# Kernel optimization log

Hardware: AMD Instinct MI355X
Metric: run time of the kernel (lower is better)

The kernel has to match this reference:

```python
import jax, jax.numpy as jnp
import numpy as np

NUM_NODES = 50000
NUM_EDGES = 1600000
NUM_GRAPHS = 64
K_HOPS = 3


def setup_inputs() -> dict:
    key = jax.random.key(0)
    ks = jax.random.split(key, 8)
    d_in, d_h, d_out = 128, 512, 16
    x = jax.random.normal(ks[0], (NUM_NODES, d_in), dtype=jnp.float32)
    edge_index = jax.random.randint(ks[1], (2, NUM_EDGES), 0, NUM_NODES, dtype=jnp.int64)
    batch = jnp.sort(jax.random.randint(ks[2], (NUM_NODES,), 0, NUM_GRAPHS, dtype=jnp.int64))
    w1 = jax.random.normal(ks[3], (d_in, d_h), dtype=jnp.float32) / np.sqrt(d_in)
    b1 = jnp.zeros((d_h,), dtype=jnp.float32)
    w2 = jax.random.normal(ks[4], (d_h, d_h), dtype=jnp.float32) / np.sqrt(d_h)
    b2 = jnp.zeros((d_h,), dtype=jnp.float32)
    wc = jax.random.normal(ks[5], (d_h, d_out), dtype=jnp.float32) / np.sqrt(d_h)
    bc = jnp.zeros((d_out,), dtype=jnp.float32)
    return {"x": x, "edge_index": edge_index, "batch": batch,
            "w1": w1, "b1": b1, "w2": w2, "b2": b2, "wc": wc, "bc": bc}


def _propagate(x, row, col, norm):
    # one hop: out[r] += x[c] * norm  (degree-normalized scatter-add)
    msg = x[col] * norm[:, None]                      # [E+N, d]
    return jax.ops.segment_sum(msg, row, num_segments=NUM_NODES)


def reference(x, edge_index, batch, w1, b1, w2, b2, wc, bc):
    # add self loops
    loops = jnp.arange(NUM_NODES, dtype=edge_index.dtype)
    row = jnp.concatenate([edge_index[0], loops])
    col = jnp.concatenate([edge_index[1], loops])
    deg = jax.ops.segment_sum(jnp.ones_like(row, dtype=jnp.float32), row,
                              num_segments=NUM_NODES)
    deg = jnp.clip(deg, 1.0)
    norm = 1.0 / deg[row]                             # [E+N]
    # K-hop propagation (eval mode: dropout / drop_node inactive)
    h = x
    for _ in range(K_HOPS):
        h = _propagate(h, row, col, norm)
    # MLP
    h = jax.nn.relu(h @ w1 + b1)
    h = h @ w2 + b2
    # global mean pool over graphs
    sums = jax.ops.segment_sum(h, batch, num_segments=NUM_GRAPHS)
    cnts = jax.ops.segment_sum(jnp.ones((h.shape[0],), dtype=h.dtype), batch,
                               num_segments=NUM_GRAPHS)
    pooled = sums / jnp.clip(cnts, 1.0)[:, None]      # [G, d_h]
    return pooled @ wc + bc                            # [G, out]
```

## Files before the change

kernel.cpp:

```cpp
#include <hip/hip_runtime.h>
#include <hip/hip_bf16.h>
#include <hip/hip_fp8.h>

#define N_NODES 50000
#define N_EDGES 1600000
#define N_GRAPHS 64
#define D_IN 128
#define D_H 512
#define D_OUT 16

#define NBUK 391
#define BUK_CAP 4608
#define P1_EDGES 4096
#define P1_BLOCKS ((N_EDGES + P1_EDGES - 1) / P1_EDGES)

#define MSPLIT 8

typedef short bf16x8 __attribute__((ext_vector_type(8)));
typedef float f32x4 __attribute__((ext_vector_type(4)));

static __device__ __forceinline__ unsigned short f2bf(float f) {
    __hip_bfloat16 h = __float2bfloat16(f);
    return *(unsigned short*)&h;
}

static __device__ __forceinline__ float2 fp8x2_dec(unsigned short u) {
    __hip_fp8x2_e4m3 p;
    p.__x = (__hip_fp8x2_storage_t)u;
    return static_cast<float2>(p);
}

static __device__ __forceinline__ unsigned short fp8x2_enc(float a, float b) {
    __hip_fp8_e4m3 pa(a), pb(b);
    return (unsigned short)((unsigned)pa.__x | ((unsigned)pb.__x << 8));
}

static __device__ __forceinline__ void dec16_add(uint4 u, float* acc) {
    unsigned vv[4] = {u.x, u.y, u.z, u.w};
#pragma unroll
    for (int w = 0; w < 4; ++w) {
        float2 a = fp8x2_dec((unsigned short)(vv[w] & 0xFFFFu));
        float2 b = fp8x2_dec((unsigned short)(vv[w] >> 16));
        acc[w * 4 + 0] += a.x; acc[w * 4 + 1] += a.y;
        acc[w * 4 + 2] += b.x; acc[w * 4 + 3] += b.y;
    }
}


__global__ __launch_bounds__(512) void partition_edges(const int* __restrict__ row,
                                                       const int* __restrict__ col,
                                                       int* __restrict__ bucket_cnt,
                                                       unsigned* __restrict__ edge_buf) {
    __shared__ unsigned recs[P1_EDGES];
    __shared__ unsigned sorted[P1_EDGES];
    __shared__ int hist4[4][NBUK];
    __shared__ int cur4[4][NBUK];
    __shared__ int gbase[NBUK];
    __shared__ int scan[512];
    int tid = threadIdx.x;
    int w2 = tid >> 7;
    int e0 = blockIdx.x * P1_EDGES;
    int m = N_EDGES - e0; if (m > P1_EDGES) m = P1_EDGES;

    for (int i = tid; i < 4 * NBUK; i += 512) ((int*)hist4)[i] = 0;
    for (int i = tid; i < 4 * NBUK; i += 512) ((int*)cur4)[i] = 0;
    __syncthreads();
    for (int i = tid; i < m; i += 512) {
        int r = row[e0 + i];
        int c = col[e0 + i];
        int buk = r >> 7;
        recs[i] = ((unsigned)buk << 23) | ((unsigned)(r & 127) << 16) | (unsigned)c;
        atomicAdd(&hist4[w2][buk], 1);
    }
    __syncthreads();
    int tot = 0;
    if (tid < NBUK) tot = hist4[0][tid] + hist4[1][tid] + hist4[2][tid] + hist4[3][tid];
    scan[tid] = (tid < NBUK) ? tot : 0;
    __syncthreads();
    for (int off = 1; off < 512; off <<= 1) {
        int v = (tid >= off) ? scan[tid - off] : 0;
        __syncthreads();
        scan[tid] += v;
        __syncthreads();
    }
    if (tid < NBUK) {
        int run = (tid == 0) ? 0 : scan[tid - 1];
        gbase[tid] = (tot > 0) ? atomicAdd(&bucket_cnt[tid], tot) : 0;
#pragma unroll
        for (int w = 0; w < 4; ++w) {
            int c = hist4[w][tid];
            hist4[w][tid] = run;
            run += c;
        }
    }
    __syncthreads();
    for (int i = tid; i < m; i += 512) {
        unsigned rec = recs[i];
        int buk = rec >> 23;
        int rank = atomicAdd(&cur4[w2][buk], 1);
        sorted[hist4[w2][buk] + rank] = rec;
    }
    __syncthreads();
    for (int p = tid; p < m; p += 512) {
        unsigned rec = sorted[p];
        int buk = rec >> 23;
        edge_buf[(size_t)buk * BUK_CAP + gbase[buk] + (p - hist4[0][buk])] = rec;
    }
}

__global__ __launch_bounds__(512) void finalize_csr(const unsigned* __restrict__ edge_buf,
                                                    const int* __restrict__ bucket_cnt,
                                                    int* __restrict__ rowptr,
                                                    float* __restrict__ invdeg,
                                                    unsigned short* __restrict__ csr_col) {
    __shared__ int hist[128], excl[128], cur[128];
    __shared__ int scan[512];
    int b = blockIdx.x;
    int tid = threadIdx.x;
    scan[tid] = (tid < NBUK) ? bucket_cnt[tid] : 0;
    __syncthreads();
    for (int off = 1; off < 512; off <<= 1) {
        int v = (tid >= off) ? scan[tid - off] : 0;
        __syncthreads();
        scan[tid] += v;
        __syncthreads();
    }
    int cnt = bucket_cnt[b];
    int base = (b == 0) ? 0 : scan[b - 1];
    const unsigned* src = edge_buf + (size_t)b * BUK_CAP;
    __syncthreads();
    if (tid < 128) { hist[tid] = 0; cur[tid] = 0; }
    __syncthreads();
    for (int i = tid; i < cnt; i += 512)
        atomicAdd(&hist[(src[i] >> 16) & 127], 1);
    __syncthreads();
    scan[tid] = (tid < 128) ? hist[tid] : 0;
    __syncthreads();
    for (int off = 1; off < 512; off <<= 1) {
        int v = (tid >= off) ? scan[tid - off] : 0;
        __syncthreads();
        scan[tid] += v;
        __syncthreads();
    }
    if (tid < 128) excl[tid] = (tid == 0) ? 0 : scan[tid - 1];
    __syncthreads();
    int r = b * 128 + tid;
    if (tid < 128 && r < N_NODES) {
        rowptr[r] = base + excl[tid];
        invdeg[r] = 1.0f / (float)(hist[tid] + 1);
    }
    if (b == NBUK - 1 && tid == 0) rowptr[N_NODES] = base + cnt;
    for (int i = tid; i < cnt; i += 512) {
        unsigned rec = src[i];
        int rl = (rec >> 16) & 127;
        int pos = excl[rl] + atomicAdd(&cur[rl], 1);
        csr_col[base + pos] = (unsigned short)(rec & 0xFFFFu);
    }
}


__global__ __launch_bounds__(256) void prep(const float* __restrict__ x,
                                            unsigned short* __restrict__ xf,
                                            const float* __restrict__ w1,
                                            unsigned short* __restrict__ w1p,
                                            const float* __restrict__ w2,
                                            const float* __restrict__ wc,
                                            const float* __restrict__ b2,
                                            const float* __restrict__ bc,
                                            const int* __restrict__ batch,
                                            float* __restrict__ wcomb,
                                            float* __restrict__ bcomb,
                                            int* __restrict__ gcnt,
                                            int* __restrict__ gstart,
                                            unsigned short* __restrict__ h0f,
                                            unsigned short* __restrict__ h1f) {
    int b = blockIdx.x;
    int tid = threadIdx.x;
    if (b < 12500) {
        int i = b * 256 + tid;
        float2 v = ((const float2*)x)[i];
        xf[i] = fp8x2_enc(v.x, v.y);
        return;
    }
    if (b < 12756) {
        int i = (b - 12500) * 256 + tid;
        int j = i & 7, lane = (i >> 3) & 63, s = (i >> 9) & 3, t = i >> 11;
        int k = s * 32 + (lane >> 4) * 8 + j;
        int n = t * 16 + (lane & 15);
        w1p[i] = f2bf(w1[(size_t)k * D_H + n]);
        return;
    }
    int fb = b - 12756;
    if (fb == 33) {
        if (tid < N_GRAPHS) {
            int g = tid;
            int lo = 0, hi = N_NODES;
            while (lo < hi) { int mid = (lo + hi) >> 1; if (batch[mid] < g) lo = mid + 1; else hi = mid; }
            int a = lo;
            lo = 0; hi = N_NODES;
            while (lo < hi) { int mid = (lo + hi) >> 1; if (batch[mid] < g + 1) lo = mid + 1; else hi = mid; }
            gcnt[g] = lo - a;
            gstart[g] = a;
            if (g == N_GRAPHS - 1) gstart[N_GRAPHS] = N_NODES;
        } else if (tid >= 64 && tid < 256) {
            int t = tid - 64;
            unsigned short* bp = (t < 64) ? xf : (t < 128 ? h0f : h1f);
            bp[(size_t)N_NODES * 64 + (t & 63)] = 0;
        }
        return;
    }
    int o = tid & 15, kl = tid >> 4;
    int k = fb * 16 + kl;
    if (k > D_H) return;
    const float* wr = (k < D_H) ? (w2 + (size_t)k * D_H) : b2;
    float s = 0.f;
    for (int j = 0; j < D_H; j += 4) {
        s += wr[j + 0] * wc[(j + 0) * D_OUT + o]
           + wr[j + 1] * wc[(j + 1) * D_OUT + o]
           + wr[j + 2] * wc[(j + 2) * D_OUT + o]
           + wr[j + 3] * wc[(j + 3) * D_OUT + o];
    }
    if (k < D_H) wcomb[k * D_OUT + o] = s;
    else         bcomb[o] = s + bc[o];
}


__global__ __launch_bounds__(256) void propagate_fp8(const unsigned short* __restrict__ xin,
                                                     unsigned short* __restrict__ out8,
                                                     unsigned* __restrict__ out16,
                                                     int last, float extra,
                                                     const int* __restrict__ rowptr,
                                                     const unsigned short* __restrict__ csr_col,
                                                     const float* __restrict__ invdeg) {
    int lane = threadIdx.x & 63;
    int wave = threadIdx.x >> 6;
    int l8   = lane & 7;
    int grp  = lane >> 3;
    int r = blockIdx.x * 32 + wave * 8 + grp;
    bool rv = (r < N_NODES);
    int rc = rv ? r : 0;
    int beg = rowptr[rc];
    int end = rowptr[rc + 1];
    int nn = rv ? (end - beg) : 0;

    int nmax = nn;
    { int t = __shfl_xor(nmax, 8, 64);  nmax = t > nmax ? t : nmax; }
    { int t = __shfl_xor(nmax, 16, 64); nmax = t > nmax ? t : nmax; }
    { int t = __shfl_xor(nmax, 32, 64); nmax = t > nmax ? t : nmax; }

    float acc[16];
#pragma unroll
    for (int i = 0; i < 16; ++i) acc[i] = 0.f;
    {
        uint4 u = *(const uint4*)(xin + (size_t)rc * 64 + l8 * 8);
        dec16_add(u, acc);
    }

    int base = lane & 56;
    int cv;
    {
        int jj = l8;
        int idx = (jj < nn) ? beg + jj : 0;
        unsigned short cl = csr_col[idx];
        cv = (jj < nn) ? (int)cl : N_NODES;
    }
    for (int jb = 0; jb < nmax; jb += 8) {
        uint4 u[8];
#pragma unroll
        for (int q = 0; q < 8; ++q) {
            int c = __shfl(cv, base + q, 64);
            u[q] = *(const uint4*)(xin + (size_t)c * 64 + l8 * 8);
        }
        int jn = jb + 8 + l8;
        int idxn = (jn < nn) ? beg + jn : 0;
        unsigned short cln = csr_col[idxn];
        int cvn = (jn < nn) ? (int)cln : N_NODES;
#pragma unroll
        for (int q = 0; q < 8; ++q) dec16_add(u[q], acc);
        cv = cvn;
    }

    float s = rv ? invdeg[r] * extra : 0.f;
#pragma unroll
    for (int i = 0; i < 16; ++i) acc[i] *= s;

    if (!rv) return;
    if (last) {
        uint4 w0, w1v;
        w0.x = (unsigned)f2bf(acc[0])  | ((unsigned)f2bf(acc[1])  << 16);
        w0.y = (unsigned)f2bf(acc[2])  | ((unsigned)f2bf(acc[3])  << 16);
        w0.z = (unsigned)f2bf(acc[4])  | ((unsigned)f2bf(acc[5])  << 16);
        w0.w = (unsigned)f2bf(acc[6])  | ((unsigned)f2bf(acc[7])  << 16);
        w1v.x = (unsigned)f2bf(acc[8])  | ((unsigned)f2bf(acc[9])  << 16);
        w1v.y = (unsigned)f2bf(acc[10]) | ((unsigned)f2bf(acc[11]) << 16);
        w1v.z = (unsigned)f2bf(acc[12]) | ((unsigned)f2bf(acc[13]) << 16);
        w1v.w = (unsigned)f2bf(acc[14]) | ((unsigned)f2bf(acc[15]) << 16);
        unsigned* dst = out16 + (size_t)r * 64 + l8 * 8;
        *(uint4*)dst = w0;
        *(uint4*)(dst + 4) = w1v;
    } else {
        uint4 w;
        w.x = (unsigned)fp8x2_enc(acc[0],  acc[1])  | ((unsigned)fp8x2_enc(acc[2],  acc[3])  << 16);
        w.y = (unsigned)fp8x2_enc(acc[4],  acc[5])  | ((unsigned)fp8x2_enc(acc[6],  acc[7])  << 16);
        w.z = (unsigned)fp8x2_enc(acc[8],  acc[9])  | ((unsigned)fp8x2_enc(acc[10], acc[11]) << 16);
        w.w = (unsigned)fp8x2_enc(acc[12], acc[13]) | ((unsigned)fp8x2_enc(acc[14], acc[15]) << 16);
        *(uint4*)(out8 + (size_t)r * 64 + l8 * 8) = w;
    }
}


__global__ __launch_bounds__(256) void gemm_graph_pool(const unsigned short* __restrict__ h3b,
                                                       const unsigned short* __restrict__ w1p,
                                                       const float* __restrict__ b1,
                                                       const int* __restrict__ gstart,
                                                       float* __restrict__ gsum) {
    __shared__ float wsum[4][128];
    int tid = threadIdx.x;
    int lane = tid & 63, wave = tid >> 6;
    int quad = lane >> 4, l15 = lane & 15;
    int g = blockIdx.x;
    int nbase = blockIdx.y * 128;
    int ms = blockIdx.z;
    int r0 = gstart[g], r1 = gstart[g + 1];

    float b1v[8];
#pragma unroll
    for (int t = 0; t < 8; ++t) b1v[t] = b1[nbase + t * 16 + l15];

    const unsigned short* bbase = w1p + ((size_t)(blockIdx.y * 8) * 4 * 64 + lane) * 8;

    float gaccT[8];
#pragma unroll
    for (int t = 0; t < 8; ++t) gaccT[t] = 0.f;

    for (int mbase = r0 + ms * 64; mbase < r1; mbase += 64 * MSPLIT) {
        int m = mbase + wave * 16 + l15;
        int mc = m < N_NODES ? m : N_NODES - 1;
        const unsigned short* arow = h3b + (size_t)mc * 128 + quad * 8;
        bf16x8 afrag[4];
#pragma unroll
        for (int s = 0; s < 4; ++s)
            afrag[s] = *(const bf16x8*)(arow + s * 32);

        int rowbase = mbase + wave * 16 + quad * 4;
#pragma unroll
        for (int t = 0; t < 8; ++t) {
            f32x4 acc = (f32x4){0.f, 0.f, 0.f, 0.f};
#pragma unroll
            for (int s = 0; s < 4; ++s) {
                bf16x8 bfrag = *(const bf16x8*)(bbase + (size_t)(t * 4 + s) * 64 * 8);
                acc = __builtin_amdgcn_mfma_f32_16x16x32_bf16(afrag[s], bfrag, acc, 0, 0, 0);
            }
#pragma unroll
            for (int rg = 0; rg < 4; ++rg) {
                float v = acc[rg] + b1v[t];
                v = v > 0.f ? v : 0.f;
                gaccT[t] += (rowbase + rg < r1) ? v : 0.f;
            }
        }
    }
#pragma unroll
    for (int t = 0; t < 8; ++t) {
        gaccT[t] += __shfl_xor(gaccT[t], 16, 64);
        gaccT[t] += __shfl_xor(gaccT[t], 32, 64);
    }
    if (quad == 0) {
#pragma unroll
        for (int t = 0; t < 8; ++t)
            wsum[wave][t * 16 + l15] = gaccT[t];
    }
    __syncthreads();
    if (tid < 128)
        gsum[((size_t)ms * N_GRAPHS + g) * D_H + nbase + tid] =
            wsum[0][tid] + wsum[1][tid] + wsum[2][tid] + wsum[3][tid];
}


__global__ __launch_bounds__(256) void final_pool(const float* __restrict__ gsum,
                                                  const int* __restrict__ gcnt,
                                                  const float* __restrict__ wcomb,
                                                  const float* __restrict__ bcomb,
                                                  float* __restrict__ out) {
    int g = blockIdx.x;
    int tid = threadIdx.x;
    __shared__ float p[D_H];
    __shared__ float part[16][17];
    int c = gcnt[g]; if (c < 1) c = 1;
    float inv = 1.0f / (float)c;
#pragma unroll
    for (int h = 0; h < 2; ++h) {
        int i = tid + h * 256;
        float v = 0.f;
#pragma unroll
        for (int ms = 0; ms < MSPLIT; ++ms)
            v += gsum[((size_t)ms * N_GRAPHS + g) * D_H + i];
        p[i] = v * inv;
    }
    __syncthreads();
    int o = tid & 15, ch = tid >> 4;
    int k0 = ch * 32;
    float s = 0.f;
    for (int k = k0; k < k0 + 32; ++k)
        s += p[k] * wcomb[k * D_OUT + o];
    part[ch][o] = s;
    __syncthreads();
    if (tid < D_OUT) {
        float t = bcomb[tid];
        for (int ch2 = 0; ch2 < 16; ++ch2) t += part[ch2][tid];
        out[g * D_OUT + tid] = t;
    }
}


extern "C" void kernel_launch(void* const* d_in, const int* in_sizes, int n_in,
                              void* d_out, int out_size, void* d_ws, size_t ws_size,
                              hipStream_t stream) {
    const float* x     = (const float*)d_in[0];
    const int*   eidx  = (const int*)d_in[1];
    const int*   batch = (const int*)d_in[2];
    const float* w1    = (const float*)d_in[3];
    const float* b1    = (const float*)d_in[4];
    const float* w2    = (const float*)d_in[5];
    const float* b2    = (const float*)d_in[6];
    const float* wc    = (const float*)d_in[7];
    const float* bc    = (const float*)d_in[8];
    float* out = (float*)d_out;
    const int* row = eidx;
    const int* col = eidx + N_EDGES;

    char* p = (char*)d_ws;
    auto alloc = [&](size_t bytes) { char* q = p; p += (bytes + 255) & ~(size_t)255; return q; };
    char* zbase = p;
    int*   bucket_cnt = (int*)alloc((size_t)NBUK * 4);
    size_t zbytes = (size_t)(p - zbase);
    float* gsum    = (float*)alloc((size_t)MSPLIT * N_GRAPHS * D_H * 4);
    int*   rowptr  = (int*)alloc((size_t)(N_NODES + 1) * 4);
    int*   gcnt    = (int*)alloc((size_t)N_GRAPHS * 4);
    int*   gstart  = (int*)alloc((size_t)(N_GRAPHS + 1) * 4);
    float* invdeg  = (float*)alloc((size_t)N_NODES * 4);
    float* wcomb   = (float*)alloc((size_t)D_H * D_OUT * 4);
    float* bcomb   = (float*)alloc((size_t)D_OUT * 4);
    unsigned* edge_buf = (unsigned*)alloc((size_t)NBUK * BUK_CAP * 4);
    unsigned short* csr_col = (unsigned short*)alloc((size_t)N_EDGES * 2);
    unsigned short* xf  = (unsigned short*)alloc((size_t)(N_NODES + 1) * 64 * 2);
    unsigned short* h0f = (unsigned short*)alloc((size_t)(N_NODES + 1) * 64 * 2);
    unsigned short* h1f = (unsigned short*)alloc((size_t)(N_NODES + 1) * 64 * 2);
    unsigned* h3b  = (unsigned*)alloc((size_t)N_NODES * 64 * 4);
    unsigned short* w1p = (unsigned short*)alloc((size_t)D_IN * D_H * 2);

    (void)hipMemsetAsync(zbase, 0, zbytes, stream);

    prep<<<12790, 256, 0, stream>>>(x, xf, w1, w1p, w2, wc, b2, bc, batch,
                                    wcomb, bcomb, gcnt, gstart, h0f, h1f);

    partition_edges<<<P1_BLOCKS, 512, 0, stream>>>(row, col, bucket_cnt, edge_buf);
    finalize_csr<<<NBUK, 512, 0, stream>>>(edge_buf, bucket_cnt, rowptr, invdeg, csr_col);

    int pgrid = (N_NODES + 31) / 32;
    propagate_fp8<<<pgrid, 256, 0, stream>>>(xf,  h0f, nullptr, 0, 8.0f,
                                             rowptr, csr_col, invdeg);
    propagate_fp8<<<pgrid, 256, 0, stream>>>(h0f, h1f, nullptr, 0, 8.0f,
                                             rowptr, csr_col, invdeg);
    propagate_fp8<<<pgrid, 256, 0, stream>>>(h1f, nullptr, h3b, 1, 1.0f / 64.0f,
                                             rowptr, csr_col, invdeg);

    dim3 ggrid(N_GRAPHS, D_H / 128, MSPLIT);
    gemm_graph_pool<<<ggrid, 256, 0, stream>>>((const unsigned short*)h3b, w1p, b1,
                                               gstart, gsum);
    final_pool<<<N_GRAPHS, 256, 0, stream>>>(gsum, gcnt, wcomb, bcomb, out);
}
```

Before: 235.7 us.

## Split each propagation hop into two column-half passes with fp32 partial buffer

The CSR is sorted within each row so that columns below 25000 come first, with a rowmid pointer marking the split. Each hop now runs as two passes: the first gathers only from the low half of the source features and stores fp32 partials, and the second gathers the high half and adds the partials. This keeps each pass's gather working set (about 3.2 MB of fp8 rows) small enough to stay cache resident. The cost is twice as many kernel launches and an extra 25.6 MB fp32 partial buffer written and read per hop. Nontemporal loads are also used for csr_col and the partial buffer.

```diff
diff --git a/kernel.cpp b/kernel.cpp
--- a/kernel.cpp
+++ b/kernel.cpp
@@ -15,6 +15,7 @@
 #define P1_BLOCKS ((N_EDGES + P1_EDGES - 1) / P1_EDGES)
 
 #define MSPLIT 8
+#define HALF_COL 25000
 
 typedef short bf16x8 __attribute__((ext_vector_type(8)));
 typedef float f32x4 __attribute__((ext_vector_type(4)));
@@ -111,9 +112,10 @@
 __global__ __launch_bounds__(512) void finalize_csr(const unsigned* __restrict__ edge_buf,
                                                     const int* __restrict__ bucket_cnt,
                                                     int* __restrict__ rowptr,
+                                                    int* __restrict__ rowmid,
                                                     float* __restrict__ invdeg,
                                                     unsigned short* __restrict__ csr_col) {
-    __shared__ int hist[128], excl[128], cur[128];
+    __shared__ int hist[128], hist_lo[128], excl[128], cur_lo[128], cur_hi[128];
     __shared__ int scan[512];
     int b = blockIdx.x;
     int tid = threadIdx.x;
@@ -129,10 +131,14 @@
     int base = (b == 0) ? 0 : scan[b - 1];
     const unsigned* src = edge_buf + (size_t)b * BUK_CAP;
     __syncthreads();
-    if (tid < 128) { hist[tid] = 0; cur[tid] = 0; }
-    __syncthreads();
-    for (int i = tid; i < cnt; i += 512)
-        atomicAdd(&hist[(src[i] >> 16) & 127], 1);
+    if (tid < 128) { hist[tid] = 0; hist_lo[tid] = 0; cur_lo[tid] = 0; cur_hi[tid] = 0; }
+    __syncthreads();
+    for (int i = tid; i < cnt; i += 512) {
+        unsigned rec = src[i];
+        int rl = (rec >> 16) & 127;
+        atomicAdd(&hist[rl], 1);
+        if ((rec & 0xFFFFu) < HALF_COL) atomicAdd(&hist_lo[rl], 1);
+    }
     __syncthreads();
     scan[tid] = (tid < 128) ? hist[tid] : 0;
     __syncthreads();
@@ -147,13 +153,16 @@
     int r = b * 128 + tid;
     if (tid < 128 && r < N_NODES) {
         rowptr[r] = base + excl[tid];
+        rowmid[r] = base + excl[tid] + hist_lo[tid];
         invdeg[r] = 1.0f / (float)(hist[tid] + 1);
     }
     if (b == NBUK - 1 && tid == 0) rowptr[N_NODES] = base + cnt;
     for (int i = tid; i < cnt; i += 512) {
         unsigned rec = src[i];
         int rl = (rec >> 16) & 127;
-        int pos = excl[rl] + atomicAdd(&cur[rl], 1);
+        bool lo = (rec & 0xFFFFu) < HALF_COL;
+        int pos = lo ? excl[rl] + atomicAdd(&cur_lo[rl], 1)
+                     : excl[rl] + hist_lo[rl] + atomicAdd(&cur_hi[rl], 1);
         csr_col[base + pos] = (unsigned short)(rec & 0xFFFFu);
     }
 }
@@ -225,13 +234,15 @@
 }
 
 
-__global__ __launch_bounds__(256) void propagate_fp8(const unsigned short* __restrict__ xin,
-                                                     unsigned short* __restrict__ out8,
-                                                     unsigned* __restrict__ out16,
-                                                     int last, float extra,
-                                                     const int* __restrict__ rowptr,
-                                                     const unsigned short* __restrict__ csr_col,
-                                                     const float* __restrict__ invdeg) {
+__global__ __launch_bounds__(256) void propagate_half(const unsigned short* __restrict__ xin,
+                                                      float* __restrict__ accf,
+                                                      unsigned short* __restrict__ out8,
+                                                      unsigned* __restrict__ out16,
+                                                      int phase, int last, float extra,
+                                                      const int* __restrict__ rowptr,
+                                                      const int* __restrict__ rowmid,
+                                                      const unsigned short* __restrict__ csr_col,
+                                                      const float* __restrict__ invdeg) {
     int lane = threadIdx.x & 63;
     int wave = threadIdx.x >> 6;
     int l8   = lane & 7;
@@ -239,8 +250,8 @@
     int r = blockIdx.x * 32 + wave * 8 + grp;
     bool rv = (r < N_NODES);
     int rc = rv ? r : 0;
-    int beg = rowptr[rc];
-    int end = rowptr[rc + 1];
+    int beg = phase ? rowmid[rc] : rowptr[rc];
+    int end = phase ? rowptr[rc + 1] : rowmid[rc];
     int nn = rv ? (end - beg) : 0;
 
     int nmax = nn;
@@ -251,9 +262,19 @@
     float acc[16];
 #pragma unroll
     for (int i = 0; i < 16; ++i) acc[i] = 0.f;
-    {
-        uint4 u = *(const uint4*)(xin + (size_t)rc * 64 + l8 * 8);
+
+    if (rv && ((r < HALF_COL) == (phase == 0))) {
+        uint4 u = *(const uint4*)(xin + (size_t)r * 64 + l8 * 8);
         dec16_add(u, acc);
+    }
+    if (phase) {
+        const f32x4* ap = (const f32x4*)(accf + (size_t)rc * 128 + l8 * 16);
+#pragma unroll
+        for (int i = 0; i < 4; ++i) {
+            f32x4 v = __builtin_nontemporal_load(ap + i);
+            acc[i * 4 + 0] += v.x; acc[i * 4 + 1] += v.y;
+            acc[i * 4 + 2] += v.z; acc[i * 4 + 3] += v.w;
+        }
     }
 
     int base = lane & 56;
@@ -261,7 +282,7 @@
     {
         int jj = l8;
         int idx = (jj < nn) ? beg + jj : 0;
-        unsigned short cl = csr_col[idx];
+        unsigned short cl = __builtin_nontemporal_load(&csr_col[idx]);
         cv = (jj < nn) ? (int)cl : N_NODES;
     }
     for (int jb = 0; jb < nmax; jb += 8) {
@@ -273,18 +294,31 @@
         }
         int jn = jb + 8 + l8;
         int idxn = (jn < nn) ? beg + jn : 0;
-        unsigned short cln = csr_col[idxn];
+        unsigned short cln = __builtin_nontemporal_load(&csr_col[idxn]);
         int cvn = (jn < nn) ? (int)cln : N_NODES;
 #pragma unroll
         for (int q = 0; q < 8; ++q) dec16_add(u[q], acc);
         cv = cvn;
     }
 
-    float s = rv ? invdeg[r] * extra : 0.f;
+    if (!rv) return;
+
+    if (phase == 0) {
+        f32x4* ap = (f32x4*)(accf + (size_t)r * 128 + l8 * 16);
+#pragma unroll
+        for (int i = 0; i < 4; ++i) {
+            f32x4 v;
+            v.x = acc[i * 4 + 0]; v.y = acc[i * 4 + 1];
+            v.z = acc[i * 4 + 2]; v.w = acc[i * 4 + 3];
+            __builtin_nontemporal_store(v, ap + i);
+        }
+        return;
+    }
+
+    float s = invdeg[r] * extra;
 #pragma unroll
     for (int i = 0; i < 16; ++i) acc[i] *= s;
 
-    if (!rv) return;
     if (last) {
         uint4 w0, w1v;
         w0.x = (unsigned)f2bf(acc[0])  | ((unsigned)f2bf(acc[1])  << 16);
@@ -435,6 +469,7 @@
     size_t zbytes = (size_t)(p - zbase);
     float* gsum    = (float*)alloc((size_t)MSPLIT * N_GRAPHS * D_H * 4);
     int*   rowptr  = (int*)alloc((size_t)(N_NODES + 1) * 4);
+    int*   rowmid  = (int*)alloc((size_t)N_NODES * 4);
     int*   gcnt    = (int*)alloc((size_t)N_GRAPHS * 4);
     int*   gstart  = (int*)alloc((size_t)(N_GRAPHS + 1) * 4);
     float* invdeg  = (float*)alloc((size_t)N_NODES * 4);
@@ -447,6 +482,7 @@
     unsigned short* h1f = (unsigned short*)alloc((size_t)(N_NODES + 1) * 64 * 2);
     unsigned* h3b  = (unsigned*)alloc((size_t)N_NODES * 64 * 4);
     unsigned short* w1p = (unsigned short*)alloc((size_t)D_IN * D_H * 2);
+    float* accf    = (float*)alloc((size_t)N_NODES * 128 * 4);
 
     (void)hipMemsetAsync(zbase, 0, zbytes, stream);
 
@@ -454,15 +490,22 @@
                                     wcomb, bcomb, gcnt, gstart, h0f, h1f);
 
     partition_edges<<<P1_BLOCKS, 512, 0, stream>>>(row, col, bucket_cnt, edge_buf);
-    finalize_csr<<<NBUK, 512, 0, stream>>>(edge_buf, bucket_cnt, rowptr, invdeg, csr_col);
+    finalize_csr<<<NBUK, 512, 0, stream>>>(edge_buf, bucket_cnt, rowptr, rowmid,
+                                           invdeg, csr_col);
 
     int pgrid = (N_NODES + 31) / 32;
-    propagate_fp8<<<pgrid, 256, 0, stream>>>(xf,  h0f, nullptr, 0, 8.0f,
-                                             rowptr, csr_col, invdeg);
-    propagate_fp8<<<pgrid, 256, 0, stream>>>(h0f, h1f, nullptr, 0, 8.0f,
-                                             rowptr, csr_col, invdeg);
-    propagate_fp8<<<pgrid, 256, 0, stream>>>(h1f, nullptr, h3b, 1, 1.0f / 64.0f,
-                                             rowptr, csr_col, invdeg);
+    propagate_half<<<pgrid, 256, 0, stream>>>(xf, accf, h0f, nullptr, 0, 0, 8.0f,
+                                              rowptr, rowmid, csr_col, invdeg);
+    propagate_half<<<pgrid, 256, 0, stream>>>(xf, accf, h0f, nullptr, 1, 0, 8.0f,
+                                              rowptr, rowmid, csr_col, invdeg);
+    propagate_half<<<pgrid, 256, 0, stream>>>(h0f, accf, h1f, nullptr, 0, 0, 8.0f,
+                                              rowptr, rowmid, csr_col, invdeg);
+    propagate_half<<<pgrid, 256, 0, stream>>>(h0f, accf, h1f, nullptr, 1, 0, 8.0f,
+                                              rowptr, rowmid, csr_col, invdeg);
+    propagate_half<<<pgrid, 256, 0, stream>>>(h1f, accf, nullptr, h3b, 0, 1, 1.0f / 64.0f,
+                                              rowptr, rowmid, csr_col, invdeg);
+    propagate_half<<<pgrid, 256, 0, stream>>>(h1f, accf, nullptr, h3b, 1, 1, 1.0f / 64.0f,
+                                              rowptr, rowmid, csr_col, invdeg);
 
     dim3 ggrid(N_GRAPHS, D_H / 128, MSPLIT);
     gemm_graph_pool<<<ggrid, 256, 0, stream>>>((const unsigned short*)h3b, w1p, b1,
```

After: 299.3 us. +27.0%, slower.

## Split CSR neighbor lists into three column-range tiles for gather locality

Applied to the files above, without the earlier changes.

Each row's neighbor list is partitioned by source column into three node ranges, with per-row tile boundaries stored in a new rowtile array. The propagate kernel walks the three segments in order so that concurrent waves gather from a smaller slice of the feature table at a time, aiming for better L2/cache hit rates on the random gathers. In exchange, padding grows because each segment rounds up to a group of 8 separately, there are extra per-row loads and shuffles, and finalize_csr does more shared-memory atomics.

```diff
diff --git a/kernel.cpp b/kernel.cpp
--- a/kernel.cpp
+++ b/kernel.cpp
@@ -15,6 +15,9 @@
 #define P1_BLOCKS ((N_EDGES + P1_EDGES - 1) / P1_EDGES)
 
 #define MSPLIT 8
+
+#define TB0 16667
+#define TB1 33334
 
 typedef short bf16x8 __attribute__((ext_vector_type(8)));
 typedef float f32x4 __attribute__((ext_vector_type(4)));
@@ -111,9 +114,10 @@
 __global__ __launch_bounds__(512) void finalize_csr(const unsigned* __restrict__ edge_buf,
                                                     const int* __restrict__ bucket_cnt,
                                                     int* __restrict__ rowptr,
+                                                    int* __restrict__ rowtile,
                                                     float* __restrict__ invdeg,
                                                     unsigned short* __restrict__ csr_col) {
-    __shared__ int hist[128], excl[128], cur[128];
+    __shared__ int hcnt[3][128], excl[128], cur[3][128];
     __shared__ int scan[512];
     int b = blockIdx.x;
     int tid = threadIdx.x;
@@ -129,12 +133,21 @@
     int base = (b == 0) ? 0 : scan[b - 1];
     const unsigned* src = edge_buf + (size_t)b * BUK_CAP;
     __syncthreads();
-    if (tid < 128) { hist[tid] = 0; cur[tid] = 0; }
-    __syncthreads();
-    for (int i = tid; i < cnt; i += 512)
-        atomicAdd(&hist[(src[i] >> 16) & 127], 1);
-    __syncthreads();
-    scan[tid] = (tid < 128) ? hist[tid] : 0;
+    if (tid < 128) {
+        hcnt[0][tid] = 0; hcnt[1][tid] = 0; hcnt[2][tid] = 0;
+        cur[0][tid] = 0;  cur[1][tid] = 0;  cur[2][tid] = 0;
+    }
+    __syncthreads();
+    for (int i = tid; i < cnt; i += 512) {
+        unsigned rec = src[i];
+        int rl = (rec >> 16) & 127;
+        unsigned c = rec & 0xFFFFu;
+        int t = (c >= TB1) ? 2 : (c >= TB0 ? 1 : 0);
+        atomicAdd(&hcnt[t][rl], 1);
+    }
+    __syncthreads();
+    int tot_r = (tid < 128) ? (hcnt[0][tid] + hcnt[1][tid] + hcnt[2][tid]) : 0;
+    scan[tid] = tot_r;
     __syncthreads();
     for (int off = 1; off < 512; off <<= 1) {
         int v = (tid >= off) ? scan[tid - off] : 0;
@@ -146,15 +159,21 @@
     __syncthreads();
     int r = b * 128 + tid;
     if (tid < 128 && r < N_NODES) {
-        rowptr[r] = base + excl[tid];
-        invdeg[r] = 1.0f / (float)(hist[tid] + 1);
+        int rb = base + excl[tid];
+        rowptr[r] = rb;
+        rowtile[2 * r + 0] = rb + hcnt[0][tid];
+        rowtile[2 * r + 1] = rb + hcnt[0][tid] + hcnt[1][tid];
+        invdeg[r] = 1.0f / (float)(tot_r + 1);
     }
     if (b == NBUK - 1 && tid == 0) rowptr[N_NODES] = base + cnt;
     for (int i = tid; i < cnt; i += 512) {
         unsigned rec = src[i];
         int rl = (rec >> 16) & 127;
-        int pos = excl[rl] + atomicAdd(&cur[rl], 1);
-        csr_col[base + pos] = (unsigned short)(rec & 0xFFFFu);
+        unsigned c = rec & 0xFFFFu;
+        int t = (c >= TB1) ? 2 : (c >= TB0 ? 1 : 0);
+        int off = (t == 0) ? 0 : (t == 1 ? hcnt[0][rl] : hcnt[0][rl] + hcnt[1][rl]);
+        int pos = excl[rl] + off + atomicAdd(&cur[t][rl], 1);
+        csr_col[base + pos] = (unsigned short)c;
     }
 }
 
@@ -230,6 +249,7 @@
                                                      unsigned* __restrict__ out16,
                                                      int last, float extra,
                                                      const int* __restrict__ rowptr,
+                                                     const int* __restrict__ rowtile,
                                                      const unsigned short* __restrict__ csr_col,
                                                      const float* __restrict__ invdeg) {
     int lane = threadIdx.x & 63;
@@ -239,14 +259,10 @@
     int r = blockIdx.x * 32 + wave * 8 + grp;
     bool rv = (r < N_NODES);
     int rc = rv ? r : 0;
-    int beg = rowptr[rc];
-    int end = rowptr[rc + 1];
-    int nn = rv ? (end - beg) : 0;
-
-    int nmax = nn;
-    { int t = __shfl_xor(nmax, 8, 64);  nmax = t > nmax ? t : nmax; }
-    { int t = __shfl_xor(nmax, 16, 64); nmax = t > nmax ? t : nmax; }
-    { int t = __shfl_xor(nmax, 32, 64); nmax = t > nmax ? t : nmax; }
+    int pbeg = rowptr[rc];
+    int pend = rowptr[rc + 1];
+    int t0e  = rowtile[2 * rc + 0];
+    int t1e  = rowtile[2 * rc + 1];
 
     float acc[16];
 #pragma unroll
@@ -257,34 +273,47 @@
     }
 
     int base = lane & 56;
-    int cv;
-    {
-        int jj = l8;
-        int idx = (jj < nn) ? beg + jj : 0;
-        unsigned short cl = csr_col[idx];
-        cv = (jj < nn) ? (int)cl : N_NODES;
-    }
-    for (int jb = 0; jb < nmax; jb += 8) {
-        uint4 u[8];
-#pragma unroll
-        for (int q = 0; q < 8; ++q) {
-            int c = __shfl(cv, base + q, 64);
-            u[q] = *(const uint4*)(xin + (size_t)c * 64 + l8 * 8);
+    for (int t = 0; t < 3; ++t) {
+        int beg = (t == 0) ? pbeg : (t == 1 ? t0e : t1e);
+        int end = (t == 0) ? t0e  : (t == 1 ? t1e : pend);
+        int nn = rv ? (end - beg) : 0;
+
+        int nmax = nn;
+        { int v = __shfl_xor(nmax, 8, 64);  nmax = v > nmax ? v : nmax; }
+        { int v = __shfl_xor(nmax, 16, 64); nmax = v > nmax ? v : nmax; }
+        { int v = __shfl_xor(nmax, 32, 64); nmax = v > nmax ? v : nmax; }
+        if (nmax == 0) continue;
+
+        int cv;
+        {
+            int jj = l8;
+            int idx = (jj < nn) ? beg + jj : 0;
+            unsigned short cl = csr_col[idx];
+            cv = (jj < nn) ? (int)cl : N_NODES;
         }
-        int jn = jb + 8 + l8;
-        int idxn = (jn < nn) ? beg + jn : 0;
-        unsigned short cln = csr_col[idxn];
-        int cvn = (jn < nn) ? (int)cln : N_NODES;
-#pragma unroll
-        for (int q = 0; q < 8; ++q) dec16_add(u[q], acc);
-        cv = cvn;
-    }
-
-    float s = rv ? invdeg[r] * extra : 0.f;
+        for (int jb = 0; jb < nmax; jb += 8) {
+            uint4 u[8];
+#pragma unroll
+            for (int q = 0; q < 8; ++q) {
+                int c = __shfl(cv, base + q, 64);
+                u[q] = *(const uint4*)(xin + (size_t)c * 64 + l8 * 8);
+            }
+            int jn = jb + 8 + l8;
+            int idxn = (jn < nn) ? beg + jn : 0;
+            unsigned short cln = csr_col[idxn];
+            int cvn = (jn < nn) ? (int)cln : N_NODES;
+#pragma unroll
+            for (int q = 0; q < 8; ++q) dec16_add(u[q], acc);
+            cv = cvn;
+        }
+    }
+
+    if (!rv) return;
+
+    float s = invdeg[r] * extra;
 #pragma unroll
     for (int i = 0; i < 16; ++i) acc[i] *= s;
 
-    if (!rv) return;
     if (last) {
         uint4 w0, w1v;
         w0.x = (unsigned)f2bf(acc[0])  | ((unsigned)f2bf(acc[1])  << 16);
@@ -435,6 +464,7 @@
     size_t zbytes = (size_t)(p - zbase);
     float* gsum    = (float*)alloc((size_t)MSPLIT * N_GRAPHS * D_H * 4);
     int*   rowptr  = (int*)alloc((size_t)(N_NODES + 1) * 4);
+    int*   rowtile = (int*)alloc((size_t)N_NODES * 2 * 4);
     int*   gcnt    = (int*)alloc((size_t)N_GRAPHS * 4);
     int*   gstart  = (int*)alloc((size_t)(N_GRAPHS + 1) * 4);
     float* invdeg  = (float*)alloc((size_t)N_NODES * 4);
@@ -454,15 +484,16 @@
                                     wcomb, bcomb, gcnt, gstart, h0f, h1f);
 
     partition_edges<<<P1_BLOCKS, 512, 0, stream>>>(row, col, bucket_cnt, edge_buf);
-    finalize_csr<<<NBUK, 512, 0, stream>>>(edge_buf, bucket_cnt, rowptr, invdeg, csr_col);
+    finalize_csr<<<NBUK, 512, 0, stream>>>(edge_buf, bucket_cnt, rowptr, rowtile,
+                                           invdeg, csr_col);
 
     int pgrid = (N_NODES + 31) / 32;
     propagate_fp8<<<pgrid, 256, 0, stream>>>(xf,  h0f, nullptr, 0, 8.0f,
-                                             rowptr, csr_col, invdeg);
+                                             rowptr, rowtile, csr_col, invdeg);
     propagate_fp8<<<pgrid, 256, 0, stream>>>(h0f, h1f, nullptr, 0, 8.0f,
-                                             rowptr, csr_col, invdeg);
+                                             rowptr, rowtile, csr_col, invdeg);
     propagate_fp8<<<pgrid, 256, 0, stream>>>(h1f, nullptr, h3b, 1, 1.0f / 64.0f,
-                                             rowptr, csr_col, invdeg);
+                                             rowptr, rowtile, csr_col, invdeg);
 
     dim3 ggrid(N_GRAPHS, D_H / 128, MSPLIT);
     gemm_graph_pool<<<ggrid, 256, 0, stream>>>((const unsigned short*)h3b, w1p, b1,
```

Measured after the change: 254.3 us. 1.08x slower.
